# Kernel optimization log

Measured on AMD Instinct MI355X. Metric: run time of the kernel, lower is better.

The kernel has to match this reference:

```python
import jax, jax.numpy as jnp
import numpy as np

B, C, H, W = 8, 256, 48, 48
CK = 64  # C // k
WSCALE = 0.3 / np.sqrt(C)  # keep exp(QK^T) finite (original has no 1/sqrt(d) scaling)


def conv1x1(x, w, b):
    # x: (B,C,H,W), w: (O,C,1,1), b: (O,) -> (B,O,H,W)
    return jnp.einsum('bchw,oc->bohw', x, w[:, :, 0, 0]) + b[None, :, None, None]


def setup_inputs() -> dict:
    key = jax.random.key(0)
    ks = jax.random.split(key, 6)
    x = jax.random.normal(ks[0], (B, C, H, W), dtype=jnp.float32)
    qw = jax.random.normal(ks[1], (CK, C, 1, 1), dtype=jnp.float32) * WSCALE
    kw = jax.random.normal(ks[2], (CK, C, 1, 1), dtype=jnp.float32) * WSCALE
    vw = jax.random.normal(ks[3], (C, C, 1, 1), dtype=jnp.float32) * (1.0 / np.sqrt(C))
    gw = jax.random.normal(ks[4], (C, C, 1, 1), dtype=jnp.float32) * (1.0 / np.sqrt(C))
    zk = jnp.zeros((CK,), dtype=jnp.float32)
    zc = jnp.zeros((C,), dtype=jnp.float32)
    return {
        'x': x,
        'query_weight': qw, 'query_bias': zk,
        'key_weight': kw, 'key_bias': zk,
        'value_weight': vw, 'value_bias': zc,
        'gamma_weight': gw, 'gamma_bias': zc,
        'k': 4,
    }


def reference(x, query_weight, query_bias, key_weight, key_bias,
              value_weight, value_bias, gamma_weight, gamma_bias, k):
    b, c, h, w = x.shape
    n = h * w
    q = conv1x1(x, query_weight, query_bias).reshape(b, -1, n)   # (B,Ck,N)
    kk = conv1x1(x, key_weight, key_bias).reshape(b, -1, n)      # (B,Ck,N)
    # energy[b,i,j] = q_i . k_j  (queries on rows, no sqrt(d) scaling)
    energy = jnp.einsum('bci,bcj->bij', q, kk)                   # (B,N,N)
    energy = jnp.exp(energy)
    energy = energy / jnp.sum(energy, axis=2, keepdims=True)     # unnormalized-softmax over keys
    v = conv1x1(x, value_weight, value_bias).reshape(b, c, n)    # (B,C,N)
    # out[b,c,j] = sum_i v[b,c,i] * energy[b,i,j]  (faithful to torch.bmm(V, energy))
    out = jnp.einsum('bci,bij->bcj', v, energy).reshape(b, c, h, w)
    out = conv1x1(out, gamma_weight, gamma_bias)
    return out
```

## Files before the change

kernel.cpp:

```cpp
#include <hip/hip_runtime.h>

#define BATCH 8
#define CIN   256
#define NPIX  2304
#define CKD   64
#define NIT   (NPIX / 16)
#define NIC   (NPIX / 32)
#define NJB   (NPIX / 64)
#define NCH   (NPIX / 64)

typedef _Float16 f16;
typedef __attribute__((ext_vector_type(4))) _Float16 f16x4;
typedef __attribute__((ext_vector_type(8))) _Float16 f16x8;
typedef __attribute__((ext_vector_type(4))) float    f32x4;


__global__ __launch_bounds__(256) void cast_w(
    const float* __restrict__ qw, const float* __restrict__ kw,
    const float* __restrict__ vw, const float* __restrict__ gw,
    f16* __restrict__ Wqk, f16* __restrict__ Wv, f16* __restrict__ Wg)
{
    int idx = (blockIdx.x * 256 + threadIdx.x) * 4;
    const float* src;
    f16* dst;
    if (idx < 16384)      { src = qw + idx;           dst = Wqk + idx; }
    else if (idx < 32768) { src = kw + (idx - 16384); dst = Wqk + idx; }
    else if (idx < 98304) { src = vw + (idx - 32768); dst = Wv + (idx - 32768); }
    else                  { src = gw + (idx - 98304); dst = Wg + (idx - 98304); }
    float4 v = *(const float4*)src;
    f16x4 h = { (f16)v.x, (f16)v.y, (f16)v.z, (f16)v.w };
    *(f16x4*)dst = h;
}

__global__ __launch_bounds__(256) void cast_xT(
    const float* __restrict__ x, f16* __restrict__ xT)
{
    __shared__ float s[64][65];
    const int t = threadIdx.x;
    const int n0 = blockIdx.x * 64, c0 = blockIdx.y * 64, b = blockIdx.z;
    const float* xb = x + ((size_t)b * CIN + c0) * NPIX + n0;

    const int cl = t >> 4, ng = (t & 15) * 4;
    #pragma unroll
    for (int p = 0; p < 4; ++p) {
        float4 v = *(const float4*)(xb + (size_t)(cl + 16 * p) * NPIX + ng);
        s[cl + 16 * p][ng + 0] = v.x;
        s[cl + 16 * p][ng + 1] = v.y;
        s[cl + 16 * p][ng + 2] = v.z;
        s[cl + 16 * p][ng + 3] = v.w;
    }
    __syncthreads();
    const int nl = t >> 2, cs = (t & 3) * 16;
    f16 h[16];
    #pragma unroll
    for (int j = 0; j < 16; ++j) h[j] = (f16)s[cs + j][nl];
    f16* gp = &xT[((size_t)b * NPIX + n0 + nl) * CIN + c0 + cs];
    *(f16x8*)gp       = *(f16x8*)&h[0];
    *(f16x8*)(gp + 8) = *(f16x8*)&h[8];
}

__global__ __launch_bounds__(256) void qk_conv_mfma(
    const f16* __restrict__ xT, const f16* __restrict__ Wqk,
    const float* __restrict__ qbias, const float* __restrict__ kbias,
    f16* __restrict__ q_blk, f16* __restrict__ k_blk)
{
    __shared__ __align__(16) f16 us[32 * 136];
    const int t = threadIdx.x, w = t >> 6, lane = t & 63;
    const int quad = lane >> 4, l16 = lane & 15;
    const int wm = w & 1, wn = w >> 1;
    const int n0 = blockIdx.x * 32, b = blockIdx.y;

    const f16* bp = xT + ((size_t)b * NPIX + n0 + 16 * wn + l16) * CIN;
    const f16* ap = Wqk + (size_t)(64 * wm + l16) * CIN;

    f32x4 acc[4];
    #pragma unroll
    for (int mt = 0; mt < 4; ++mt) acc[mt] = (f32x4){0.f, 0.f, 0.f, 0.f};

    #pragma unroll
    for (int kk = 0; kk < CIN; kk += 32) {
        f16x8 bf = *(const f16x8*)(bp + kk + quad * 8);
        #pragma unroll
        for (int mt = 0; mt < 4; ++mt) {
            f16x8 af = *(const f16x8*)(ap + (size_t)mt * 16 * CIN + kk + quad * 8);
            acc[mt] = __builtin_amdgcn_mfma_f32_16x16x32_f16(af, bf, acc[mt], 0, 0, 0);
        }
    }
    const float* bias = wm ? kbias - 64 : qbias;
    #pragma unroll
    for (int mt = 0; mt < 4; ++mt) {
        int ob = 64 * wm + 16 * mt + quad * 4;
        #pragma unroll
        for (int r = 0; r < 4; ++r)
            us[(16 * wn + l16) * 136 + ob + r] = (f16)(acc[mt][r] + bias[ob + r]);
    }
    __syncthreads();
    {
        int ks2 = t >> 7, nt = (t >> 6) & 1, ln = t & 63;
        const f16* usr = &us[(nt * 16 + (ln & 15)) * 136 + ks2 * 32 + (ln >> 4) * 8];
        size_t base = (((size_t)b * NIT + (n0 >> 4) + nt) * 2 + ks2) * 512 + ln * 8;
        *(f16x8*)&q_blk[base] = *(const f16x8*)(usr);
        *(f16x8*)&k_blk[base] = *(const f16x8*)(usr + 64);
    }
}

#define ESL 136
__global__ __launch_bounds__(256) void energy_S(
    const f16* __restrict__ q_blk, const f16* __restrict__ k_blk,
    float* __restrict__ Pred)
{
    __shared__ __align__(16) f16 es[64 * ESL];
    __shared__ float red2[2][128];
    const int t    = threadIdx.x;
    const int w    = t >> 6, lane = t & 63;
    const int quad = lane >> 4, l16 = lane & 15;
    const int j0 = blockIdx.x * 64, i0 = blockIdx.y * 128, b = blockIdx.z;
    const size_t ln8 = (size_t)lane * 8;
    const f16* qb = q_blk + (size_t)b * NIT * 2 * 512 + ln8;

    f32x4 acc[8];
    #pragma unroll
    for (int mt = 0; mt < 8; ++mt) acc[mt] = (f32x4){0.f, 0.f, 0.f, 0.f};

    #pragma unroll
    for (int ks = 0; ks < 2; ++ks) {
        f16x8 bf = *(const f16x8*)(k_blk +
            (((size_t)b * NIT + (j0 >> 4) + w) * 2 + ks) * 512 + ln8);
        #pragma unroll
        for (int mt = 0; mt < 8; ++mt) {
            f16x8 af = *(const f16x8*)(qb + ((size_t)((i0 >> 4) + mt) * 2 + ks) * 512);
            acc[mt] = __builtin_amdgcn_mfma_f32_16x16x32_f16(af, bf, acc[mt], 0, 0, 0);
        }
    }

    #pragma unroll
    for (int mt = 0; mt < 8; ++mt) {
        f16x4 h = { (f16)__expf(acc[mt][0]), (f16)__expf(acc[mt][1]),
                    (f16)__expf(acc[mt][2]), (f16)__expf(acc[mt][3]) };
        *(f16x4*)&es[(16 * w + l16) * ESL + 16 * mt + quad * 4] = h;
    }
    __syncthreads();
    {
        int i = t & 127, jq = t >> 7;
        float s = 0.f;
        #pragma unroll
        for (int jj = 0; jj < 32; ++jj)
            s += (float)es[(jq * 32 + jj) * ESL + i];
        red2[jq][i] = s;
    }
    __syncthreads();
    if (t < 128)
        Pred[((size_t)blockIdx.x * BATCH + b) * NPIX + i0 + t] =
            red2[0][t] + red2[1][t];
}

__global__ __launch_bounds__(256) void reduce_S(
    const float* __restrict__ Pred, float* __restrict__ S)
{
    const size_t BN = (size_t)BATCH * NPIX;
    size_t idx = (size_t)blockIdx.x * 256 + threadIdx.x;
    float s = 0.f;
    #pragma unroll
    for (int jb = 0; jb < NJB; ++jb)
        s += Pred[(size_t)jb * BN + idx];
    S[idx] = s;
}

__global__ __launch_bounds__(256) void v_conv_mfma(
    const f16* __restrict__ xT, const f16* __restrict__ Wv,
    const float* __restrict__ vbias, const float* __restrict__ S,
    f16* __restrict__ u_blk)
{
    __shared__ __align__(16) f16 smem[9216];
    f16* As = smem;
    f16* Bs = smem + 128 * 40;
    f16* us = smem;
    const int t = threadIdx.x, w = t >> 6, lane = t & 63;
    const int quad = lane >> 4, l16 = lane & 15;
    const int wm = w & 1, wn = w >> 1;
    const int i0 = blockIdx.x * 64, c0 = blockIdx.y * 128, b = blockIdx.z;
    const int sub = t >> 2, le = t & 3;
    const f16* srcA = Wv + (size_t)(c0 + sub) * CIN + le * 8;
    const f16* srcB = xT + ((size_t)b * NPIX + i0 + sub) * CIN + le * 8;
    const int ldsw = sub * 40 + le * 8;

    f32x4 acc[4][2];
    #pragma unroll
    for (int mt = 0; mt < 4; ++mt)
        #pragma unroll
        for (int nt = 0; nt < 2; ++nt)
            acc[mt][nt] = (f32x4){0.f, 0.f, 0.f, 0.f};

    for (int kk = 0; kk < CIN; kk += 32) {
        f16x8 ta0 = *(const f16x8*)(srcA + kk);
        f16x8 ta1 = *(const f16x8*)(srcA + (size_t)64 * CIN + kk);
        f16x8 tb0 = *(const f16x8*)(srcB + kk);
        __syncthreads();
        *(f16x8*)&As[ldsw]           = ta0;
        *(f16x8*)&As[64 * 40 + ldsw] = ta1;
        *(f16x8*)&Bs[ldsw]           = tb0;
        __syncthreads();
        f16x8 af[4], bf[2];
        #pragma unroll
        for (int mt = 0; mt < 4; ++mt)
            af[mt] = *(const f16x8*)&As[(64 * wm + 16 * mt + l16) * 40 + quad * 8];
        #pragma unroll
        for (int nt = 0; nt < 2; ++nt)
            bf[nt] = *(const f16x8*)&Bs[(32 * wn + 16 * nt + l16) * 40 + quad * 8];
        #pragma unroll
        for (int mt = 0; mt < 4; ++mt)
            #pragma unroll
            for (int nt = 0; nt < 2; ++nt)
                acc[mt][nt] = __builtin_amdgcn_mfma_f32_16x16x32_f16(
                    af[mt], bf[nt], acc[mt][nt], 0, 0, 0);
    }

    __syncthreads();
    #pragma unroll
    for (int nt = 0; nt < 2; ++nt) {
        int i = 32 * wn + 16 * nt + l16;
        float is = 1.0f / S[(size_t)b * NPIX + i0 + i];
        #pragma unroll
        for (int mt = 0; mt < 4; ++mt)
            #pragma unroll
            for (int r = 0; r < 4; ++r) {
                int c = 64 * wm + 16 * mt + quad * 4 + r;
                us[c * 72 + i] = (f16)((acc[mt][nt][r] + vbias[c0 + c]) * is);
            }
    }
    __syncthreads();
    #pragma unroll
    for (int p = 0; p < 4; ++p) {
        int g  = t + 256 * p;
        int ct = g >> 7, ic = (g >> 6) & 1, ln = g & 63;
        f16x8 v = *(const f16x8*)&us[(ct * 16 + (ln & 15)) * 72 + ic * 32 + (ln >> 4) * 8];
        *(f16x8*)&u_blk[(((size_t)b * 16 + (c0 >> 4) + ct) * NIC + (i0 >> 5) + ic) * 512 + ln * 8] = v;
    }
}

__global__ __launch_bounds__(512, 4) void fused_bmm(
    const f16* __restrict__ q_blk, const f16* __restrict__ k_blk,
    const f16* __restrict__ u_blk, f16* __restrict__ o1T)
{
    __shared__ __align__(16) f16 es[2][8][512];
    const int t = threadIdx.x, w = t >> 6, lane = t & 63;
    const int quad = lane >> 4, l16 = lane & 15;
    const int bid = blockIdx.x;
    const int b  = bid & 7;
    const int j0 = (bid >> 3) * 64;
    const size_t ln8 = (size_t)lane * 8;

    const f16* qb = q_blk + (size_t)b * NIT * 2 * 512 + ln8;
    const f16* ub = u_blk + (size_t)b * 16 * NIC * 512 + ln8;

    const int iw = w >> 1;
    const int jh = w & 1;

    f16x8 kf[2][2];
    #pragma unroll
    for (int jj = 0; jj < 2; ++jj)
        #pragma unroll
        for (int ks = 0; ks < 2; ++ks)
            kf[jj][ks] = *(const f16x8*)(k_blk +
                (((size_t)b * NIT + (j0 >> 4) + jh + 2 * jj) * 2 + ks) * 512 + ln8);

    const int CT0 = w * 2;
    const int woff = ((iw & 1) * 2 + (quad >> 1)) * 128 + l16 * 8 + (quad & 1) * 4;
    const int et0 = jh * 2 + (iw >> 1);
    const int et1 = (jh + 2) * 2 + (iw >> 1);

    f32x4 acc[2][4];
    #pragma unroll
    for (int mt = 0; mt < 2; ++mt)
        #pragma unroll
        for (int jt = 0; jt < 4; ++jt)
            acc[mt][jt] = (f32x4){0.f, 0.f, 0.f, 0.f};

#define QLD(ic, ks)  (*(const f16x8*)(qb + ((size_t)((ic) * 4 + iw) * 2 + (ks)) * 512))
#define ULD(ct, ic, is) (*(const f16x8*)(ub + ((size_t)(CT0 + (ct)) * NIC + (ic) * 2 + (is)) * 512))

#define STAGE1(q0, q1, buf) do {                                              \
    f32x4 e0 = (f32x4){0.f, 0.f, 0.f, 0.f};                                   \
    f32x4 e1 = (f32x4){0.f, 0.f, 0.f, 0.f};                                   \
    e0 = __builtin_amdgcn_mfma_f32_16x16x32_f16(q0, kf[0][0], e0, 0, 0, 0);   \
    e0 = __builtin_amdgcn_mfma_f32_16x16x32_f16(q1, kf[0][1], e0, 0, 0, 0);   \
    e1 = __builtin_amdgcn_mfma_f32_16x16x32_f16(q0, kf[1][0], e1, 0, 0, 0);   \
    e1 = __builtin_amdgcn_mfma_f32_16x16x32_f16(q1, kf[1][1], e1, 0, 0, 0);   \
    f16x4 h0 = { (f16)__expf(e0[0]), (f16)__expf(e0[1]),                      \
                 (f16)__expf(e0[2]), (f16)__expf(e0[3]) };                    \
    f16x4 h1 = { (f16)__expf(e1[0]), (f16)__expf(e1[1]),                      \
                 (f16)__expf(e1[2]), (f16)__expf(e1[3]) };                    \
    *(f16x4*)&es[buf][et0][woff] = h0;                                        \
    *(f16x4*)&es[buf][et1][woff] = h1;                                        \
} while (0)

#define STAGE2(buf, u00, u01, u10, u11) do {                                  \
    _Pragma("unroll")                                                         \
    for (int jt = 0; jt < 4; ++jt) {                                          \
        f16x8 bf0 = *(const f16x8*)&es[buf][jt * 2 + 0][ln8];                 \
        acc[0][jt] = __builtin_amdgcn_mfma_f32_16x16x32_f16(u00, bf0, acc[0][jt], 0, 0, 0); \
        acc[1][jt] = __builtin_amdgcn_mfma_f32_16x16x32_f16(u10, bf0, acc[1][jt], 0, 0, 0); \
        f16x8 bf1 = *(const f16x8*)&es[buf][jt * 2 + 1][ln8];                 \
        acc[0][jt] = __builtin_amdgcn_mfma_f32_16x16x32_f16(u01, bf1, acc[0][jt], 0, 0, 0); \
        acc[1][jt] = __builtin_amdgcn_mfma_f32_16x16x32_f16(u11, bf1, acc[1][jt], 0, 0, 0); \
    }                                                                         \
} while (0)

#define BAR() do {                                                            \
    asm volatile("s_waitcnt lgkmcnt(0)" ::: "memory");                        \
    __builtin_amdgcn_s_barrier();                                             \
} while (0)

    f16x8 qA0 = QLD(0, 0), qA1 = QLD(0, 1);
    f16x8 uA0 = ULD(0, 0, 0), uA1 = ULD(0, 0, 1);
    f16x8 uA2 = ULD(1, 0, 0), uA3 = ULD(1, 0, 1);
    f16x8 qB0 = QLD(1, 0), qB1 = QLD(1, 1);
    STAGE1(qA0, qA1, 0);
    BAR();

    f16x8 uB0, uB1, uB2, uB3;
    for (int ic = 0; ic < NCH; ic += 2) {
        const int i1 = ic + 1;
        const int i2 = (ic + 2 < NCH) ? ic + 2 : NCH - 1;
        const int i3 = (ic + 3 < NCH) ? ic + 3 : NCH - 1;
        uB0 = ULD(0, i1, 0); uB1 = ULD(0, i1, 1);
        uB2 = ULD(1, i1, 0); uB3 = ULD(1, i1, 1);
        qA0 = QLD(i2, 0); qA1 = QLD(i2, 1);
        STAGE2(0, uA0, uA1, uA2, uA3);
        STAGE1(qB0, qB1, 1);
        BAR();
        uA0 = ULD(0, i2, 0); uA1 = ULD(0, i2, 1);
        uA2 = ULD(1, i2, 0); uA3 = ULD(1, i2, 1);
        qB0 = QLD(i3, 0); qB1 = QLD(i3, 1);
        STAGE2(1, uB0, uB1, uB2, uB3);
        if (ic + 2 < NCH) STAGE1(qA0, qA1, 0);
        BAR();
    }

#undef QLD
#undef ULD
#undef STAGE1
#undef STAGE2
#undef BAR

    #pragma unroll
    for (int mt = 0; mt < 2; ++mt) {
        int cb = 32 * w + 16 * mt + quad * 4;
        #pragma unroll
        for (int jt = 0; jt < 4; ++jt) {
            int j = j0 + 16 * jt + l16;
            f16x4 h2 = { (f16)acc[mt][jt][0], (f16)acc[mt][jt][1],
                         (f16)acc[mt][jt][2], (f16)acc[mt][jt][3] };
            *(f16x4*)&o1T[((size_t)b * NPIX + j) * CIN + cb] = h2;
        }
    }
}

__global__ __launch_bounds__(256) void gamma_conv_mfma(
    const f16* __restrict__ o1T, const f16* __restrict__ Wg,
    const float* __restrict__ gbias, float* __restrict__ out)
{
    __shared__ __align__(16) f16 As[128 * 40];
    __shared__ __align__(16) f16 Bs[64 * 40];
    const int t = threadIdx.x, w = t >> 6, lane = t & 63;
    const int quad = lane >> 4, l16 = lane & 15;
    const int wm = w & 1, wn = w >> 1;
    const int j0 = blockIdx.x * 64, o0 = blockIdx.y * 128, b = blockIdx.z;
    const int sub = t >> 2, le = t & 3;
    const f16* srcA = Wg + (size_t)(o0 + sub) * CIN + le * 8;
    const f16* srcB = o1T + ((size_t)b * NPIX + j0 + sub) * CIN + le * 8;
    const int ldsw = sub * 40 + le * 8;

    f32x4 acc[4][2];
    #pragma unroll
    for (int mt = 0; mt < 4; ++mt)
        #pragma unroll
        for (int nt = 0; nt < 2; ++nt)
            acc[mt][nt] = (f32x4){0.f, 0.f, 0.f, 0.f};

    for (int kk = 0; kk < CIN; kk += 32) {
        f16x8 ta0 = *(const f16x8*)(srcA + kk);
        f16x8 ta1 = *(const f16x8*)(srcA + (size_t)64 * CIN + kk);
        f16x8 tb0 = *(const f16x8*)(srcB + kk);
        __syncthreads();
        *(f16x8*)&As[ldsw]           = ta0;
        *(f16x8*)&As[64 * 40 + ldsw] = ta1;
        *(f16x8*)&Bs[ldsw]           = tb0;
        __syncthreads();
        f16x8 af[4], bf[2];
        #pragma unroll
        for (int mt = 0; mt < 4; ++mt)
            af[mt] = *(const f16x8*)&As[(64 * wm + 16 * mt + l16) * 40 + quad * 8];
        #pragma unroll
        for (int nt = 0; nt < 2; ++nt)
            bf[nt] = *(const f16x8*)&Bs[(32 * wn + 16 * nt + l16) * 40 + quad * 8];
        #pragma unroll
        for (int mt = 0; mt < 4; ++mt)
            #pragma unroll
            for (int nt = 0; nt < 2; ++nt)
                acc[mt][nt] = __builtin_amdgcn_mfma_f32_16x16x32_f16(
                    af[mt], bf[nt], acc[mt][nt], 0, 0, 0);
    }

    #pragma unroll
    for (int mt = 0; mt < 4; ++mt)
        #pragma unroll
        for (int r = 0; r < 4; ++r) {
            int o = o0 + 64 * wm + 16 * mt + quad * 4 + r;
            float bv = gbias[o];
            #pragma unroll
            for (int nt = 0; nt < 2; ++nt) {
                int j = j0 + 32 * wn + 16 * nt + l16;
                out[((size_t)b * CIN + o) * NPIX + j] = acc[mt][nt][r] + bv;
            }
        }
}

extern "C" void kernel_launch(void* const* d_in, const int* in_sizes, int n_in,
                              void* d_out, int out_size, void* d_ws, size_t ws_size,
                              hipStream_t stream) {
    const float* x   = (const float*)d_in[0];
    const float* qw  = (const float*)d_in[1];
    const float* qbv = (const float*)d_in[2];
    const float* kw  = (const float*)d_in[3];
    const float* kbv = (const float*)d_in[4];
    const float* vw  = (const float*)d_in[5];
    const float* vbv = (const float*)d_in[6];
    const float* gw  = (const float*)d_in[7];
    const float* gbv = (const float*)d_in[8];
    float* out = (float*)d_out;

    const size_t BCN  = (size_t)BATCH * CIN * NPIX;
    const size_t BN   = (size_t)BATCH * NPIX;
    const size_t BNCK = (size_t)BATCH * NPIX * CKD;

    f16* q_blk = (f16*)d_ws;
    f16* k_blk = q_blk + BNCK;
    f16* u_blk = k_blk + BNCK;
    f16* xT    = u_blk + BCN;
    f16* o1T   = xT + BCN;
    f16* Wqk   = o1T + BCN;
    f16* Wv    = Wqk + 128 * 256;
    f16* Wg    = Wv + 256 * 256;
    float* S   = (float*)(Wg + 256 * 256);
    float* Pred= S + BN;

    cast_w<<<160, 256, 0, stream>>>(qw, kw, vw, gw, Wqk, Wv, Wg);
    cast_xT<<<dim3(NPIX / 64, CIN / 64, BATCH), 256, 0, stream>>>(x, xT);
    qk_conv_mfma<<<dim3(NPIX / 32, BATCH), 256, 0, stream>>>(xT, Wqk, qbv, kbv, q_blk, k_blk);
    energy_S<<<dim3(NPIX / 64, NPIX / 128, BATCH), 256, 0, stream>>>(q_blk, k_blk, Pred);
    reduce_S<<<(int)(BN / 256), 256, 0, stream>>>(Pred, S);
    v_conv_mfma<<<dim3(NPIX / 64, CIN / 128, BATCH), 256, 0, stream>>>(xT, Wv, vbv, S, u_blk);
    fused_bmm<<<NJB * BATCH, 512, 0, stream>>>(q_blk, k_blk, u_blk, o1T);
    gamma_conv_mfma<<<dim3(NPIX / 64, CIN / 128, BATCH), 256, 0, stream>>>(o1T, Wg, gbv, out);
}
```

Measured before the change: 192.0 us.

## Split fused_bmm reduction over i into two halves and sum in gamma conv

The fused attention bmm kernel now splits the reduction over source pixels into two halves, launching twice as many blocks. Each half writes a separate fp16 partial output, reusing the xT buffer for the second half. The gamma conv adds the two partials while loading. s_setprio is also raised around the MFMA stage. This targets low occupancy from only 288 blocks, at the cost of an extra fp16 partial write and read, and some precision loss from summing in fp16.

```diff
diff --git a/kernel.cpp b/kernel.cpp
--- a/kernel.cpp
+++ b/kernel.cpp
@@ -240,14 +240,19 @@
 
 __global__ __launch_bounds__(512, 4) void fused_bmm(
     const f16* __restrict__ q_blk, const f16* __restrict__ k_blk,
-    const f16* __restrict__ u_blk, f16* __restrict__ o1T)
+    const f16* __restrict__ u_blk, f16* __restrict__ o1A, f16* __restrict__ o1B)
 {
     __shared__ __align__(16) f16 es[2][8][512];
     const int t = threadIdx.x, w = t >> 6, lane = t & 63;
     const int quad = lane >> 4, l16 = lane & 15;
     const int bid = blockIdx.x;
-    const int b  = bid & 7;
-    const int j0 = (bid >> 3) * 64;
+    const int b   = bid & 7;
+    const int r   = bid >> 3;
+    const int j0  = (r >> 1) * 64;
+    const int half = r & 1;
+    const int ic0 = half * (NCH / 2);
+    const int icN = ic0 + NCH / 2;
+    f16* __restrict__ o1h = half ? o1B : o1A;
     const size_t ln8 = (size_t)lane * 8;
 
     const f16* qb = q_blk + (size_t)b * NIT * 2 * 512 + ln8;
@@ -295,6 +300,7 @@
 } while (0)
 
 #define STAGE2(buf, u00, u01, u10, u11) do {                                  \
+    __builtin_amdgcn_s_setprio(1);                                            \
     _Pragma("unroll")                                                         \
     for (int jt = 0; jt < 4; ++jt) {                                          \
         f16x8 bf0 = *(const f16x8*)&es[buf][jt * 2 + 0][ln8];                 \
@@ -304,6 +310,7 @@
         acc[0][jt] = __builtin_amdgcn_mfma_f32_16x16x32_f16(u01, bf1, acc[0][jt], 0, 0, 0); \
         acc[1][jt] = __builtin_amdgcn_mfma_f32_16x16x32_f16(u11, bf1, acc[1][jt], 0, 0, 0); \
     }                                                                         \
+    __builtin_amdgcn_s_setprio(0);                                            \
 } while (0)
 
 #define BAR() do {                                                            \
@@ -311,18 +318,18 @@
     __builtin_amdgcn_s_barrier();                                             \
 } while (0)
 
-    f16x8 qA0 = QLD(0, 0), qA1 = QLD(0, 1);
-    f16x8 uA0 = ULD(0, 0, 0), uA1 = ULD(0, 0, 1);
-    f16x8 uA2 = ULD(1, 0, 0), uA3 = ULD(1, 0, 1);
-    f16x8 qB0 = QLD(1, 0), qB1 = QLD(1, 1);
+    f16x8 qA0 = QLD(ic0, 0), qA1 = QLD(ic0, 1);
+    f16x8 uA0 = ULD(0, ic0, 0), uA1 = ULD(0, ic0, 1);
+    f16x8 uA2 = ULD(1, ic0, 0), uA3 = ULD(1, ic0, 1);
+    f16x8 qB0 = QLD(ic0 + 1, 0), qB1 = QLD(ic0 + 1, 1);
     STAGE1(qA0, qA1, 0);
     BAR();
 
     f16x8 uB0, uB1, uB2, uB3;
-    for (int ic = 0; ic < NCH; ic += 2) {
+    for (int ic = ic0; ic < icN; ic += 2) {
         const int i1 = ic + 1;
-        const int i2 = (ic + 2 < NCH) ? ic + 2 : NCH - 1;
-        const int i3 = (ic + 3 < NCH) ? ic + 3 : NCH - 1;
+        const int i2 = (ic + 2 < icN) ? ic + 2 : icN - 1;
+        const int i3 = (ic + 3 < icN) ? ic + 3 : icN - 1;
         uB0 = ULD(0, i1, 0); uB1 = ULD(0, i1, 1);
         uB2 = ULD(1, i1, 0); uB3 = ULD(1, i1, 1);
         qA0 = QLD(i2, 0); qA1 = QLD(i2, 1);
@@ -333,7 +340,7 @@
         uA2 = ULD(1, i2, 0); uA3 = ULD(1, i2, 1);
         qB0 = QLD(i3, 0); qB1 = QLD(i3, 1);
         STAGE2(1, uB0, uB1, uB2, uB3);
-        if (ic + 2 < NCH) STAGE1(qA0, qA1, 0);
+        if (ic + 2 < icN) STAGE1(qA0, qA1, 0);
         BAR();
     }
 
@@ -351,13 +358,14 @@
             int j = j0 + 16 * jt + l16;
             f16x4 h2 = { (f16)acc[mt][jt][0], (f16)acc[mt][jt][1],
                          (f16)acc[mt][jt][2], (f16)acc[mt][jt][3] };
-            *(f16x4*)&o1T[((size_t)b * NPIX + j) * CIN + cb] = h2;
+            *(f16x4*)&o1h[((size_t)b * NPIX + j) * CIN + cb] = h2;
         }
     }
 }
 
 __global__ __launch_bounds__(256) void gamma_conv_mfma(
-    const f16* __restrict__ o1T, const f16* __restrict__ Wg,
+    const f16* __restrict__ o1A, const f16* __restrict__ o1B,
+    const f16* __restrict__ Wg,
     const float* __restrict__ gbias, float* __restrict__ out)
 {
     __shared__ __align__(16) f16 As[128 * 40];
@@ -367,8 +375,10 @@
     const int wm = w & 1, wn = w >> 1;
     const int j0 = blockIdx.x * 64, o0 = blockIdx.y * 128, b = blockIdx.z;
     const int sub = t >> 2, le = t & 3;
-    const f16* srcA = Wg + (size_t)(o0 + sub) * CIN + le * 8;
-    const f16* srcB = o1T + ((size_t)b * NPIX + j0 + sub) * CIN + le * 8;
+    const f16* srcA  = Wg + (size_t)(o0 + sub) * CIN + le * 8;
+    const size_t boff = ((size_t)b * NPIX + j0 + sub) * CIN + le * 8;
+    const f16* srcB  = o1A + boff;
+    const f16* srcB2 = o1B + boff;
     const int ldsw = sub * 40 + le * 8;
 
     f32x4 acc[4][2];
@@ -382,6 +392,8 @@
         f16x8 ta0 = *(const f16x8*)(srcA + kk);
         f16x8 ta1 = *(const f16x8*)(srcA + (size_t)64 * CIN + kk);
         f16x8 tb0 = *(const f16x8*)(srcB + kk);
+        f16x8 tb1 = *(const f16x8*)(srcB2 + kk);
+        tb0 = tb0 + tb1;
         __syncthreads();
         *(f16x8*)&As[ldsw]           = ta0;
         *(f16x8*)&As[64 * 40 + ldsw] = ta1;
@@ -451,6 +463,6 @@
     energy_S<<<dim3(NPIX / 64, NPIX / 128, BATCH), 256, 0, stream>>>(q_blk, k_blk, Pred);
     reduce_S<<<(int)(BN / 256), 256, 0, stream>>>(Pred, S);
     v_conv_mfma<<<dim3(NPIX / 64, CIN / 128, BATCH), 256, 0, stream>>>(xT, Wv, vbv, S, u_blk);
-    fused_bmm<<<NJB * BATCH, 512, 0, stream>>>(q_blk, k_blk, u_blk, o1T);
-    gamma_conv_mfma<<<dim3(NPIX / 64, CIN / 128, BATCH), 256, 0, stream>>>(o1T, Wg, gbv, out);
-}
+    fused_bmm<<<NJB * BATCH * 2, 512, 0, stream>>>(q_blk, k_blk, u_blk, o1T, xT);
+    gamma_conv_mfma<<<dim3(NPIX / 64, CIN / 128, BATCH), 256, 0, stream>>>(o1T, xT, Wg, gbv, out);
+}
```

Measured after the change: 192.8 us. Within noise of the previous version (+0.4%).
